# Kernel tuning notes

Measured on AMD Instinct MI355X. Metric: run time of the kernel, lower is better.

## Reference

```python
import jax, jax.numpy as jnp
import numpy as np

N_NODES = 100000


def _gcn_conv(x, W, b, src, dst, ew, num_nodes):
    # PyG GCNConv: symmetric normalization with self-loops already included
    # in (src, dst, ew). deg computed on destination (col) index.
    deg = jax.ops.segment_sum(ew, dst, num_segments=num_nodes)  # [N]
    dinv = jnp.where(deg > 0, jax.lax.rsqrt(deg), 0.0)          # [N]
    norm = dinv[src] * ew * dinv[dst]                           # [E]
    h = x @ W                                                   # [N, out]
    msg = h[src] * norm[:, None]                                # [E, out] gather+scale
    out = jax.ops.segment_sum(msg, dst, num_segments=num_nodes) # scatter-add
    return out + b


def setup_inputs() -> dict:
    key = jax.random.key(0)
    k = jax.random.split(key, 8)
    in_c, hid_c, out_c = 128, 128, 64
    E, EL = 1600000, 200000
    x = jax.random.normal(k[0], (N_NODES, in_c), dtype=jnp.float32)
    edge_index = jax.random.randint(k[1], (2, E), 0, N_NODES, dtype=jnp.int64)
    edge_weight = jax.random.uniform(k[2], (E,), dtype=jnp.float32)
    edge_label_index = jax.random.randint(k[3], (2, EL), 0, N_NODES, dtype=jnp.int64)
    # Glorot-ish params
    W1 = jax.random.normal(k[4], (in_c, hid_c), dtype=jnp.float32) / np.sqrt(in_c)
    b1 = jnp.zeros((hid_c,), dtype=jnp.float32)
    W2 = jax.random.normal(k[5], (hid_c, out_c), dtype=jnp.float32) / np.sqrt(hid_c)
    b2 = jnp.zeros((out_c,), dtype=jnp.float32)
    return {"x": x, "edge_index": edge_index, "edge_weight": edge_weight,
            "edge_label_index": edge_label_index,
            "W1": W1, "b1": b1, "W2": W2, "b2": b2}


def reference(x, edge_index, edge_weight, edge_label_index, W1, b1, W2, b2):
    n = x.shape[0]
    # add self-loops (weight 1.0), static shape
    loop = jnp.arange(n, dtype=edge_index.dtype)
    src = jnp.concatenate([edge_index[0], loop])
    dst = jnp.concatenate([edge_index[1], loop])
    ew = jnp.concatenate([edge_weight, jnp.ones((n,), dtype=edge_weight.dtype)])
    h = jax.nn.relu(_gcn_conv(x, W1, b1, src, dst, ew, n))
    z = _gcn_conv(h, W2, b2, src, dst, ew, n)          # [N, out_c]
    # decode: edge dot-product
    return (z[edge_label_index[0]] * z[edge_label_index[1]]).sum(axis=-1)
```

## Files before the change

### kernel.cpp

```cpp
#include <hip/hip_runtime.h>
#include <hip/hip_fp16.h>
#include <math.h>

__device__ __forceinline__ float2 h2f2(unsigned int u) {
    __half2 h = *reinterpret_cast<__half2*>(&u);
    return __half22float2(h);
}
__device__ __forceinline__ unsigned int f2h2(float a, float b) {
    __half2 h = __floats2half2_rn(a, b);
    return *reinterpret_cast<unsigned int*>(&h);
}

__global__ __launch_bounds__(256) void gemm128_hist_kernel(
        const float* __restrict__ X, const float* __restrict__ W, __half* __restrict__ Y, int n,
        const int* __restrict__ dst, int* __restrict__ cnt, int* __restrict__ rank, int E) {
    constexpr int CG  = 32;
    constexpr int M   = 64;
    constexpr int RT  = 8;
    constexpr int KC  = 32;
    constexpr int LDX = 132;
    __shared__ float  Xl[M * LDX];
    __shared__ float4 Wl[KC * CG];

    const int bid = blockIdx.x;
    const int t = threadIdx.x;
    const int EPB = (E + (int)gridDim.x - 1) / (int)gridDim.x;
    const int eBeg = bid * EPB;
    const int eEnd = min(eBeg + EPB, E);

    if ((bid & 1) == 0) {
        for (int e = eBeg + t; e < eEnd; e += 256)
            rank[e] = atomicAdd(&cnt[dst[e]], 1);
    }

    int row0 = bid * M;
    {
        const float4* Xg = (const float4*)X;
        for (int f = t; f < M * 32; f += 256) {
            int r = f >> 5, c4 = f & 31;
            int gr = row0 + r;
            float4 v = make_float4(0.f, 0.f, 0.f, 0.f);
            if (gr < n) v = Xg[(size_t)gr * 32 + c4];
            *(float4*)&Xl[r * LDX + c4 * 4] = v;
        }
    }

    int cg = t % CG;
    int r0 = (t / CG) * RT;

    float4 acc[RT];
#pragma unroll
    for (int r = 0; r < RT; r++) acc[r] = make_float4(0.f, 0.f, 0.f, 0.f);

    const float4* Wg = (const float4*)W;
    for (int kc = 0; kc < 128; kc += KC) {
        __syncthreads();
        for (int f = t; f < KC * CG; f += 256)
            Wl[f] = Wg[(size_t)kc * CG + f];
        __syncthreads();
#pragma unroll 4
        for (int k = 0; k < KC; k += 4) {
            float4 b0 = Wl[(k + 0) * CG + cg];
            float4 b1 = Wl[(k + 1) * CG + cg];
            float4 b2 = Wl[(k + 2) * CG + cg];
            float4 b3 = Wl[(k + 3) * CG + cg];
#pragma unroll
            for (int r = 0; r < RT; r++) {
                float4 a = *(float4*)&Xl[(r0 + r) * LDX + kc + k];
                acc[r].x += a.x * b0.x + a.y * b1.x + a.z * b2.x + a.w * b3.x;
                acc[r].y += a.x * b0.y + a.y * b1.y + a.z * b2.y + a.w * b3.y;
                acc[r].z += a.x * b0.z + a.y * b1.z + a.z * b2.z + a.w * b3.z;
                acc[r].w += a.x * b0.w + a.y * b1.w + a.z * b2.w + a.w * b3.w;
            }
        }
    }

#pragma unroll
    for (int r = 0; r < RT; r++) {
        int gr = row0 + r0 + r;
        if (gr < n) {
            uint2 u = make_uint2(f2h2(acc[r].x, acc[r].y), f2h2(acc[r].z, acc[r].w));
            *(uint2*)&Y[(size_t)gr * 128 + cg * 4] = u;
        }
    }

    if (bid & 1) {
        for (int e = eBeg + t; e < eEnd; e += 256)
            rank[e] = atomicAdd(&cnt[dst[e]], 1);
    }
}

__global__ __launch_bounds__(256) void scan_block(const int* __restrict__ in, int* __restrict__ out,
                                                  int* __restrict__ bsum, int n) {
    __shared__ int s[256];
    int tid = threadIdx.x;
    int base = blockIdx.x * 1024 + tid * 4;
    int a0 = (base + 0 < n) ? in[base + 0] : 0;
    int a1 = (base + 1 < n) ? in[base + 1] : 0;
    int a2 = (base + 2 < n) ? in[base + 2] : 0;
    int a3 = (base + 3 < n) ? in[base + 3] : 0;
    int tsum = a0 + a1 + a2 + a3;
    s[tid] = tsum;
    __syncthreads();
    for (int off = 1; off < 256; off <<= 1) {
        int v = (tid >= off) ? s[tid - off] : 0;
        __syncthreads();
        s[tid] += v;
        __syncthreads();
    }
    int texcl = s[tid] - tsum;
    if (base + 0 < n) out[base + 0] = texcl;
    if (base + 1 < n) out[base + 1] = texcl + a0;
    if (base + 2 < n) out[base + 2] = texcl + a0 + a1;
    if (base + 3 < n) out[base + 3] = texcl + a0 + a1 + a2;
    if (tid == 255) bsum[blockIdx.x] = s[255];
}

__global__ __launch_bounds__(256) void scan_bsums(int* __restrict__ bsum, int nb) {
    __shared__ int s[256];
    __shared__ int carry_s;
    int tid = threadIdx.x;
    if (tid == 0) carry_s = 0;
    __syncthreads();
    for (int base = 0; base < nb; base += 256) {
        int v = (base + tid < nb) ? bsum[base + tid] : 0;
        int orig = v;
        s[tid] = v;
        __syncthreads();
        for (int off = 1; off < 256; off <<= 1) {
            int u = (tid >= off) ? s[tid - off] : 0;
            __syncthreads();
            s[tid] += u;
            __syncthreads();
        }
        int carry = carry_s;
        int excl = s[tid] - orig + carry;
        if (base + tid < nb) bsum[base + tid] = excl;
        int tot = s[255];
        __syncthreads();
        if (tid == 0) carry_s = carry + tot;
        __syncthreads();
    }
}

__global__ void scan_add(int* __restrict__ rowptr, const int* __restrict__ bscan, int n) {
    int t = blockIdx.x * blockDim.x + threadIdx.x;
    if (t < n) rowptr[t] += bscan[t >> 10];
}

__global__ void scatter_pairs(const int* __restrict__ src, const int* __restrict__ dst,
                              const float* __restrict__ ew, const int* __restrict__ rowptr,
                              const int* __restrict__ rank, int2* __restrict__ pairs, int E) {
    int e = blockIdx.x * blockDim.x + threadIdx.x;
    if (e >= E) return;
    int d = dst[e];
    int p = rowptr[d] + rank[e];
    pairs[p] = make_int2(src[e], __float_as_int(ew[e]));
}

__global__ void deg_dinv_kernel(const int2* __restrict__ pairs, const int* __restrict__ rowptr,
                                float* __restrict__ dinv, int n) {
    int i = blockIdx.x * blockDim.x + threadIdx.x;
    if (i >= n) return;
    int beg = rowptr[i], end = rowptr[i + 1];
    float s = 0.f;
    for (int j = beg; j < end; j++) s += __int_as_float(pairs[j].y);
    dinv[i] = 1.0f / sqrtf(s + 1.0f);
}

__global__ void premul_kernel(int2* __restrict__ pairs, const float* __restrict__ dinv, int E) {
    int e = blockIdx.x * blockDim.x + threadIdx.x;
    if (e >= E) return;
    int2 p = pairs[e];
    p.y = __float_as_int(__int_as_float(p.y) * dinv[p.x]);
    pairs[e] = p;
}

__global__ __launch_bounds__(512, 4) void gather_mv_kernel(const __half* __restrict__ H,
                                                           const int* __restrict__ rowptr,
                                                           const int2* __restrict__ pairs,
                                                           const float* __restrict__ dinv,
                                                           const float* __restrict__ bias,
                                                           const float* __restrict__ W2,
                                                           __half* __restrict__ Z, int n) {
    __shared__ float h1s[16 * 128];
    __shared__ float w2s[128 * 64];
    const int t = threadIdx.x;
    const int nl = t >> 5;
    const int c4 = t & 31;
    const int node = blockIdx.x * 16 + nl;

    {
        const float4* W2g = (const float4*)W2;
        float4* w2s4 = (float4*)w2s;
#pragma unroll
        for (int f = 0; f < 4; f++) w2s4[f * 512 + t] = W2g[f * 512 + t];
    }

    float4 acc[4];
#pragma unroll
    for (int i = 0; i < 4; i++) acc[i] = make_float4(0.f, 0.f, 0.f, 0.f);

    float di = 0.f;
    int beg = 0, end = 0;
    if (node < n) {
        beg = rowptr[node]; end = rowptr[node + 1];
        di = dinv[node];
        uint2 hv = *(const uint2*)&H[(size_t)node * 128 + c4 * 4];
        float2 f01 = h2f2(hv.x), f23 = h2f2(hv.y);
        acc[0].x = f01.x * di; acc[0].y = f01.y * di;
        acc[0].z = f23.x * di; acc[0].w = f23.y * di;
    }

    if (beg < end) {
        int2 pc[8];
#pragma unroll
        for (int i = 0; i < 8; i++) {
            int jj = beg + i;
            pc[i] = pairs[jj < end ? jj : beg];
        }
        for (int j = beg; j < end; j += 8) {
            uint2 v[8];
#pragma unroll
            for (int i = 0; i < 8; i++)
                v[i] = *(const uint2*)&H[(size_t)(unsigned)pc[i].x * 128 + c4 * 4];
            int2 pn[8];
            int jn = j + 8;
#pragma unroll
            for (int i = 0; i < 8; i++) {
                int jj = jn + i;
                pn[i] = pairs[jj < end ? jj : beg];
            }
#pragma unroll
            for (int i = 0; i < 8; i++) {
                float w = (j + i < end) ? __int_as_float(pc[i].y) : 0.f;
                float2 g01 = h2f2(v[i].x), g23 = h2f2(v[i].y);
                acc[i & 3].x += g01.x * w; acc[i & 3].y += g01.y * w;
                acc[i & 3].z += g23.x * w; acc[i & 3].w += g23.y * w;
            }
#pragma unroll
            for (int i = 0; i < 8; i++) pc[i] = pn[i];
        }
    }

    float4 a0 = make_float4(0.f, 0.f, 0.f, 0.f);
    if (node < n) {
        float4 bb = ((const float4*)bias)[c4];
        a0.x = fmaxf(((acc[0].x + acc[1].x) + (acc[2].x + acc[3].x)) * di + bb.x, 0.f);
        a0.y = fmaxf(((acc[0].y + acc[1].y) + (acc[2].y + acc[3].y)) * di + bb.y, 0.f);
        a0.z = fmaxf(((acc[0].z + acc[1].z) + (acc[2].z + acc[3].z)) * di + bb.z, 0.f);
        a0.w = fmaxf(((acc[0].w + acc[1].w) + (acc[2].w + acc[3].w)) * di + bb.w, 0.f);
    }
    *(float4*)&h1s[nl * 128 + c4 * 4] = a0;
    __syncthreads();

    float z0 = 0.f, z1 = 0.f;
    const float* hrow = &h1s[nl * 128];
    const float2* w2c = (const float2*)w2s;
#pragma unroll 8
    for (int k = 0; k < 128; k++) {
        float hk = hrow[k];
        float2 w = w2c[k * 32 + c4];
        z0 += hk * w.x;
        z1 += hk * w.y;
    }
    if (node < n) *(unsigned int*)&Z[(size_t)node * 64 + c4 * 2] = f2h2(z0, z1);
}

__global__ __launch_bounds__(256, 4) void gather_reduce64(const __half* __restrict__ H,
                                                          const int* __restrict__ rowptr,
                                                          const int2* __restrict__ pairs,
                                                          const float* __restrict__ dinv,
                                                          const float* __restrict__ bias,
                                                          __half* __restrict__ out, int n) {
    constexpr int TPN = 16;
    int t = blockIdx.x * blockDim.x + threadIdx.x;
    int node = t / TPN;
    int c4 = t % TPN;
    if (node >= n) return;
    int beg = rowptr[node], end = rowptr[node + 1];
    float di = dinv[node];
    float4 bb = ((const float4*)bias)[c4];
    float4 acc[4];
    {
        uint2 hv = *(const uint2*)&H[(size_t)node * 64 + c4 * 4];
        float2 f01 = h2f2(hv.x), f23 = h2f2(hv.y);
        acc[0].x = f01.x * di; acc[0].y = f01.y * di;
        acc[0].z = f23.x * di; acc[0].w = f23.y * di;
    }
#pragma unroll
    for (int i = 1; i < 4; i++) acc[i] = make_float4(0.f, 0.f, 0.f, 0.f);

    if (beg < end) {
        int2 pc[8];
#pragma unroll
        for (int i = 0; i < 8; i++) {
            int jj = beg + i;
            pc[i] = pairs[jj < end ? jj : beg];
        }
        for (int j = beg; j < end; j += 8) {
            uint2 v[8];
#pragma unroll
            for (int i = 0; i < 8; i++)
                v[i] = *(const uint2*)&H[(size_t)(unsigned)pc[i].x * 64 + c4 * 4];
            int2 pn[8];
            int jn = j + 8;
#pragma unroll
            for (int i = 0; i < 8; i++) {
                int jj = jn + i;
                pn[i] = pairs[jj < end ? jj : beg];
            }
#pragma unroll
            for (int i = 0; i < 8; i++) {
                float w = (j + i < end) ? __int_as_float(pc[i].y) : 0.f;
                float2 g01 = h2f2(v[i].x), g23 = h2f2(v[i].y);
                acc[i & 3].x += g01.x * w; acc[i & 3].y += g01.y * w;
                acc[i & 3].z += g23.x * w; acc[i & 3].w += g23.y * w;
            }
#pragma unroll
            for (int i = 0; i < 8; i++) pc[i] = pn[i];
        }
    }

    float4 r;
    r.x = ((acc[0].x + acc[1].x) + (acc[2].x + acc[3].x)) * di + bb.x;
    r.y = ((acc[0].y + acc[1].y) + (acc[2].y + acc[3].y)) * di + bb.y;
    r.z = ((acc[0].z + acc[1].z) + (acc[2].z + acc[3].z)) * di + bb.z;
    r.w = ((acc[0].w + acc[1].w) + (acc[2].w + acc[3].w)) * di + bb.w;
    uint2 u = make_uint2(f2h2(r.x, r.y), f2h2(r.z, r.w));
    *(uint2*)&out[(size_t)node * 64 + c4 * 4] = u;
}

__global__ void decode_kernel(const __half* __restrict__ Z, const int* __restrict__ ea,
                              const int* __restrict__ eb, float* __restrict__ out, int L) {
    int t = blockIdx.x * blockDim.x + threadIdx.x;
    int e = t >> 4;
    int c = (t & 15) << 2;
    if (e >= L) return;
    uint2 ua = *(const uint2*)&Z[(size_t)ea[e] * 64 + c];
    uint2 ub = *(const uint2*)&Z[(size_t)eb[e] * 64 + c];
    float2 a01 = h2f2(ua.x), a23 = h2f2(ua.y);
    float2 b01 = h2f2(ub.x), b23 = h2f2(ub.y);
    float p = a01.x * b01.x + a01.y * b01.y + a23.x * b23.x + a23.y * b23.y;
    p += __shfl_xor(p, 1);
    p += __shfl_xor(p, 2);
    p += __shfl_xor(p, 4);
    p += __shfl_xor(p, 8);
    if ((t & 15) == 0) out[e] = p;
}

extern "C" void kernel_launch(void* const* d_in, const int* in_sizes, int n_in,
                              void* d_out, int out_size, void* d_ws, size_t ws_size,
                              hipStream_t stream) {
    const float* x   = (const float*)d_in[0];
    const int*   ei  = (const int*)d_in[1];
    const float* ew  = (const float*)d_in[2];
    const int*   eli = (const int*)d_in[3];
    const float* W1  = (const float*)d_in[4];
    const float* b1  = (const float*)d_in[5];
    const float* W2  = (const float*)d_in[6];
    const float* b2  = (const float*)d_in[7];
    float* out = (float*)d_out;

    const int N = in_sizes[0] / 128;
    const int E = in_sizes[2];
    const int L = in_sizes[3] / 2;
    const int NP = ((N + 255) / 256) * 256;

    float* ws     = (float*)d_ws;
    float* dinv   = ws;
    int*   cnt    = (int*)(ws + NP);
    int*   rowptr = cnt + NP;
    int*   bsum   = rowptr + NP;
    int*   rank   = bsum + 1024;
    int2*  pairs  = (int2*)(rank + E);
    __half* A     = (__half*)(pairs + E);
    __half* B     = (__half*)((float*)(pairs + E) + (size_t)NP * 128);
    __half* Zf    = A;

    const int n1 = N + 1;
    const int nb = (n1 + 1023) / 1024;

    hipMemsetAsync(cnt, 0, (size_t)n1 * 4, stream);

    const int Gg = (N + 63) / 64;
    gemm128_hist_kernel<<<Gg, 256, 0, stream>>>(x, W1, A, N, ei + E, cnt, rank, E);

    scan_block<<<nb, 256, 0, stream>>>(cnt, rowptr, bsum, n1);
    scan_bsums<<<1, 256, 0, stream>>>(bsum, nb);
    scan_add<<<(n1 + 255) / 256, 256, 0, stream>>>(rowptr, bsum, n1);
    scatter_pairs<<<(E + 255) / 256, 256, 0, stream>>>(ei, ei + E, ew, rowptr, rank, pairs, E);
    deg_dinv_kernel<<<(N + 255) / 256, 256, 0, stream>>>(pairs, rowptr, dinv, N);
    premul_kernel<<<(E + 255) / 256, 256, 0, stream>>>(pairs, dinv, E);

    gather_mv_kernel<<<(N + 15) / 16, 512, 0, stream>>>(A, rowptr, pairs, dinv, b1, W2, B, N);

    gather_reduce64<<<(N * 16 + 255) / 256, 256, 0, stream>>>(B, rowptr, pairs, dinv, b2, Zf, N);

    decode_kernel<<<(L * 16 + 255) / 256, 256, 0, stream>>>(Zf, eli, eli + L, out, L);
}
```

Baseline: 421.8 us.

## Use packed fp16 dot2 for W2 matvec and decode, simplify gather addressing

The fused gather+matvec kernel now stores the hidden row and W2 in shared memory as packed half2 values and computes the 128x64 matvec with v_dot2 fp16 instructions, halving LDS footprint and the inner loop count. The decode kernel uses fdot2 as well. Gather loads switch to 32-bit byte-offset addressing with explicit fmaf accumulation. This lowers LDS usage, which may raise occupancy, and cuts ALU work, at the cost of rounding the post-ReLU hidden activations and W2 to fp16.

```diff
diff --git a/kernel.cpp b/kernel.cpp
--- a/kernel.cpp
+++ b/kernel.cpp
@@ -2,13 +2,15 @@
 #include <hip/hip_fp16.h>
 #include <math.h>
 
-__device__ __forceinline__ float2 h2f2(unsigned int u) {
-    __half2 h = *reinterpret_cast<__half2*>(&u);
-    return __half22float2(h);
-}
+typedef _Float16 f16x2 __attribute__((ext_vector_type(2)));
+
+__device__ __forceinline__ f16x2 u2h(unsigned int u) { return __builtin_bit_cast(f16x2, u); }
 __device__ __forceinline__ unsigned int f2h2(float a, float b) {
     __half2 h = __floats2half2_rn(a, b);
     return *reinterpret_cast<unsigned int*>(&h);
+}
+__device__ __forceinline__ float fdot2h(unsigned int a, unsigned int b, float c) {
+    return __builtin_amdgcn_fdot2(u2h(a), u2h(b), c, false);
 }
 
 __global__ __launch_bounds__(256) void gemm128_hist_kernel(
@@ -183,18 +185,21 @@
                                                            const float* __restrict__ bias,
                                                            const float* __restrict__ W2,
                                                            __half* __restrict__ Z, int n) {
-    __shared__ float h1s[16 * 128];
-    __shared__ float w2s[128 * 64];
+    __shared__ unsigned h1s2[16 * 64];
+    __shared__ unsigned w2p[64 * 64];
     const int t = threadIdx.x;
     const int nl = t >> 5;
     const int c4 = t & 31;
     const int node = blockIdx.x * 16 + nl;
+    const unsigned coff = (unsigned)c4 * 8u;
 
     {
-        const float4* W2g = (const float4*)W2;
-        float4* w2s4 = (float4*)w2s;
-#pragma unroll
-        for (int f = 0; f < 4; f++) w2s4[f * 512 + t] = W2g[f * 512 + t];
+#pragma unroll
+        for (int f = 0; f < 8; f++) {
+            int idx = f * 512 + t;
+            int kp = idx >> 6, c = idx & 63;
+            w2p[idx] = f2h2(W2[(2 * kp) * 64 + c], W2[(2 * kp + 1) * 64 + c]);
+        }
     }
 
     float4 acc[4];
@@ -206,10 +211,10 @@
     if (node < n) {
         beg = rowptr[node]; end = rowptr[node + 1];
         di = dinv[node];
-        uint2 hv = *(const uint2*)&H[(size_t)node * 128 + c4 * 4];
-        float2 f01 = h2f2(hv.x), f23 = h2f2(hv.y);
-        acc[0].x = f01.x * di; acc[0].y = f01.y * di;
-        acc[0].z = f23.x * di; acc[0].w = f23.y * di;
+        uint2 hv = *(const uint2*)((const char*)H + (size_t)(((unsigned)node << 8) + coff));
+        f16x2 ha = u2h(hv.x), hb = u2h(hv.y);
+        acc[0].x = (float)ha.x * di; acc[0].y = (float)ha.y * di;
+        acc[0].z = (float)hb.x * di; acc[0].w = (float)hb.y * di;
     }
 
     if (beg < end) {
@@ -223,7 +228,7 @@
             uint2 v[8];
 #pragma unroll
             for (int i = 0; i < 8; i++)
-                v[i] = *(const uint2*)&H[(size_t)(unsigned)pc[i].x * 128 + c4 * 4];
+                v[i] = *(const uint2*)((const char*)H + (size_t)(((unsigned)pc[i].x << 8) + coff));
             int2 pn[8];
             int jn = j + 8;
 #pragma unroll
@@ -234,35 +239,39 @@
 #pragma unroll
             for (int i = 0; i < 8; i++) {
                 float w = (j + i < end) ? __int_as_float(pc[i].y) : 0.f;
-                float2 g01 = h2f2(v[i].x), g23 = h2f2(v[i].y);
-                acc[i & 3].x += g01.x * w; acc[i & 3].y += g01.y * w;
-                acc[i & 3].z += g23.x * w; acc[i & 3].w += g23.y * w;
+                f16x2 ga = u2h(v[i].x), gb = u2h(v[i].y);
+                acc[i & 3].x = fmaf((float)ga.x, w, acc[i & 3].x);
+                acc[i & 3].y = fmaf((float)ga.y, w, acc[i & 3].y);
+                acc[i & 3].z = fmaf((float)gb.x, w, acc[i & 3].z);
+                acc[i & 3].w = fmaf((float)gb.y, w, acc[i & 3].w);
             }
 #pragma unroll
             for (int i = 0; i < 8; i++) pc[i] = pn[i];
         }
     }
 
-    float4 a0 = make_float4(0.f, 0.f, 0.f, 0.f);
-    if (node < n) {
-        float4 bb = ((const float4*)bias)[c4];
-        a0.x = fmaxf(((acc[0].x + acc[1].x) + (acc[2].x + acc[3].x)) * di + bb.x, 0.f);
-        a0.y = fmaxf(((acc[0].y + acc[1].y) + (acc[2].y + acc[3].y)) * di + bb.y, 0.f);
-        a0.z = fmaxf(((acc[0].z + acc[1].z) + (acc[2].z + acc[3].z)) * di + bb.z, 0.f);
-        a0.w = fmaxf(((acc[0].w + acc[1].w) + (acc[2].w + acc[3].w)) * di + bb.w, 0.f);
-    }
-    *(float4*)&h1s[nl * 128 + c4 * 4] = a0;
+    {
+        float4 a0 = make_float4(0.f, 0.f, 0.f, 0.f);
+        if (node < n) {
+            float4 bb = ((const float4*)bias)[c4];
+            a0.x = fmaxf(((acc[0].x + acc[1].x) + (acc[2].x + acc[3].x)) * di + bb.x, 0.f);
+            a0.y = fmaxf(((acc[0].y + acc[1].y) + (acc[2].y + acc[3].y)) * di + bb.y, 0.f);
+            a0.z = fmaxf(((acc[0].z + acc[1].z) + (acc[2].z + acc[3].z)) * di + bb.z, 0.f);
+            a0.w = fmaxf(((acc[0].w + acc[1].w) + (acc[2].w + acc[3].w)) * di + bb.w, 0.f);
+        }
+        h1s2[nl * 64 + c4 * 2 + 0] = f2h2(a0.x, a0.y);
+        h1s2[nl * 64 + c4 * 2 + 1] = f2h2(a0.z, a0.w);
+    }
     __syncthreads();
 
     float z0 = 0.f, z1 = 0.f;
-    const float* hrow = &h1s[nl * 128];
-    const float2* w2c = (const float2*)w2s;
+    const unsigned* hrow = &h1s2[nl * 64];
 #pragma unroll 8
-    for (int k = 0; k < 128; k++) {
-        float hk = hrow[k];
-        float2 w = w2c[k * 32 + c4];
-        z0 += hk * w.x;
-        z1 += hk * w.y;
+    for (int kp = 0; kp < 64; kp++) {
+        unsigned h = hrow[kp];
+        uint2 wv = *(const uint2*)&w2p[kp * 64 + c4 * 2];
+        z0 = fdot2h(h, wv.x, z0);
+        z1 = fdot2h(h, wv.y, z1);
     }
     if (node < n) *(unsigned int*)&Z[(size_t)node * 64 + c4 * 2] = f2h2(z0, z1);
 }
@@ -278,15 +287,16 @@
     int node = t / TPN;
     int c4 = t % TPN;
     if (node >= n) return;
+    const unsigned coff = (unsigned)c4 * 8u;
     int beg = rowptr[node], end = rowptr[node + 1];
     float di = dinv[node];
     float4 bb = ((const float4*)bias)[c4];
     float4 acc[4];
     {
-        uint2 hv = *(const uint2*)&H[(size_t)node * 64 + c4 * 4];
-        float2 f01 = h2f2(hv.x), f23 = h2f2(hv.y);
-        acc[0].x = f01.x * di; acc[0].y = f01.y * di;
-        acc[0].z = f23.x * di; acc[0].w = f23.y * di;
+        uint2 hv = *(const uint2*)((const char*)H + (size_t)(((unsigned)node << 7) + coff));
+        f16x2 ha = u2h(hv.x), hb = u2h(hv.y);
+        acc[0].x = (float)ha.x * di; acc[0].y = (float)ha.y * di;
+        acc[0].z = (float)hb.x * di; acc[0].w = (float)hb.y * di;
     }
 #pragma unroll
     for (int i = 1; i < 4; i++) acc[i] = make_float4(0.f, 0.f, 0.f, 0.f);
@@ -302,7 +312,7 @@
             uint2 v[8];
 #pragma unroll
             for (int i = 0; i < 8; i++)
-                v[i] = *(const uint2*)&H[(size_t)(unsigned)pc[i].x * 64 + c4 * 4];
+                v[i] = *(const uint2*)((const char*)H + (size_t)(((unsigned)pc[i].x << 7) + coff));
             int2 pn[8];
             int jn = j + 8;
 #pragma unroll
@@ -313,9 +323,11 @@
 #pragma unroll
             for (int i = 0; i < 8; i++) {
                 float w = (j + i < end) ? __int_as_float(pc[i].y) : 0.f;
-                float2 g01 = h2f2(v[i].x), g23 = h2f2(v[i].y);
-                acc[i & 3].x += g01.x * w; acc[i & 3].y += g01.y * w;
-                acc[i & 3].z += g23.x * w; acc[i & 3].w += g23.y * w;
+                f16x2 ga = u2h(v[i].x), gb = u2h(v[i].y);
+                acc[i & 3].x = fmaf((float)ga.x, w, acc[i & 3].x);
+                acc[i & 3].y = fmaf((float)ga.y, w, acc[i & 3].y);
+                acc[i & 3].z = fmaf((float)gb.x, w, acc[i & 3].z);
+                acc[i & 3].w = fmaf((float)gb.y, w, acc[i & 3].w);
             }
 #pragma unroll
             for (int i = 0; i < 8; i++) pc[i] = pn[i];
@@ -339,9 +351,7 @@
     if (e >= L) return;
     uint2 ua = *(const uint2*)&Z[(size_t)ea[e] * 64 + c];
     uint2 ub = *(const uint2*)&Z[(size_t)eb[e] * 64 + c];
-    float2 a01 = h2f2(ua.x), a23 = h2f2(ua.y);
-    float2 b01 = h2f2(ub.x), b23 = h2f2(ub.y);
-    float p = a01.x * b01.x + a01.y * b01.y + a23.x * b23.x + a23.y * b23.y;
+    float p = fdot2h(ua.x, ub.x, fdot2h(ua.y, ub.y, 0.f));
     p += __shfl_xor(p, 1);
     p += __shfl_xor(p, 2);
     p += __shfl_xor(p, 4);
```

Result: faster. 406.0 us (-3.7%).
